# Kernel optimization log

Hardware: AMD Instinct MI355X
Metric: run time of the kernel (lower is better)

## Reference

```python
import jax, jax.numpy as jnp
import numpy as np
from jax import lax

B, C, H, W, K = 64, 64, 128, 128, 4
EPS = 1e-5

def setup_inputs() -> dict:
    key = jax.random.key(0)
    ks = jax.random.split(key, 8)
    def p(i, shape, scale=0.05):
        return jax.random.normal(ks[i], shape, dtype=jnp.float32) * scale
    return {
        "rgb":   jax.random.normal(ks[0], (B, C, H, W), dtype=jnp.float32),
        "depth": jax.random.normal(ks[1], (B, C, H, W), dtype=jnp.float32),
        # kernel_gen MLP: Linear(2C->C), Linear(C -> K*C*9)
        "w1": p(2, (C, 2 * C)), "b1": jnp.zeros((C,), jnp.float32),
        "w2": p(3, (K * C * 9, C)), "b2": jnp.zeros((K * C * 9,), jnp.float32),
        # freq_decompose: Conv3x3(C->C) + BN (eval-mode stats)
        "fd_w": p(4, (C, C, 3, 3)), "fd_b": jnp.zeros((C,), jnp.float32),
        "fd_scale": jnp.ones((C,), jnp.float32), "fd_bias": jnp.zeros((C,), jnp.float32),
        "fd_mean": jnp.zeros((C,), jnp.float32), "fd_var": jnp.ones((C,), jnp.float32),
        # fusion: Conv1x1(2C->C) + BN
        "fu_w": p(5, (C, 2 * C, 1, 1)), "fu_b": jnp.zeros((C,), jnp.float32),
        "fu_scale": jnp.ones((C,), jnp.float32), "fu_bias": jnp.zeros((C,), jnp.float32),
        "fu_mean": jnp.zeros((C,), jnp.float32), "fu_var": jnp.ones((C,), jnp.float32),
    }

def _bn(x, scale, bias, mean, var):
    # eval-mode batchnorm over channel axis 1
    inv = scale / jnp.sqrt(var + EPS)
    return x * inv[None, :, None, None] + (bias - mean * inv)[None, :, None, None]

def _conv(x, w, pad):
    return lax.conv_general_dilated(x, w, (1, 1), ((pad, pad), (pad, pad)),
                                    dimension_numbers=("NCHW", "OIHW", "NCHW"))

def reference(rgb, depth, w1, b1, w2, b2,
              fd_w, fd_b, fd_scale, fd_bias, fd_mean, fd_var,
              fu_w, fu_b, fu_scale, fu_bias, fu_mean, fu_var):
    b, c, h, w = rgb.shape
    k = w2.shape[0] // (c * 9)
    # kernel generation: global avg pool over concat -> MLP
    pooled = jnp.concatenate([rgb, depth], axis=1).mean(axis=(2, 3))  # [B, 2C]
    hid = jax.nn.relu(pooled @ w1.T + b1)                             # [B, C]
    kernels = (hid @ w2.T + b2).reshape(b, k, c, 3, 3)                # [B, K, C, 3, 3]
    norms = jnp.linalg.norm(kernels.reshape(b, k, -1), axis=2)        # [B, K]
    attn = jax.nn.softmax(norms, axis=1)
    weighted_kernel = jnp.einsum("bk,bkcij->bcij", attn, kernels)     # [B, C, 3, 3]
    # NOTE: faithful to the torch code: plain conv2d with out_channels=B (requires B==C)
    dynamic_feat = _conv(rgb, weighted_kernel, 1)                     # [B, B, H, W]
    freq_feat = jax.nn.relu(_bn(_conv(depth, fd_w, 1) + fd_b[None, :, None, None],
                                fd_scale, fd_bias, fd_mean, fd_var))
    cat = jnp.concatenate([dynamic_feat, freq_feat], axis=1)          # [B, 2C, H, W]
    fused = jax.nn.relu(_bn(_conv(cat, fu_w, 0) + fu_b[None, :, None, None],
                            fu_scale, fu_bias, fu_mean, fu_var))
    return fused
```

## Files before the change

### kernel.cpp

```cpp
#include <hip/hip_runtime.h>
#include <hip/hip_bf16.h>

#define CB 64
#define HH 128
#define WW 128
#define KK 4
#define EPSV 1e-5f
#define HWSZ (HH*WW)

using f32x4   = __attribute__((ext_vector_type(4))) float;
using f32x16  = __attribute__((ext_vector_type(16))) float;
using short8  = __attribute__((ext_vector_type(8))) short;

static constexpr size_t WS_POOLED = 0;
static constexpr size_t WS_HID    = 8192;
static constexpr size_t WS_KERN   = 12288;
static constexpr size_t WS_SSQ    = 159744;
static constexpr size_t WS_WK     = 160000;
static constexpr size_t WS_EFFW   = 196864;
static constexpr size_t WS_FUW2   = 233728;
static constexpr size_t WS_FDINV  = 237824;
static constexpr size_t WS_FDBETA = 237888;
static constexpr size_t WS_FUINV  = 237952;
static constexpr size_t WS_FUBETA = 238016;
static constexpr size_t WT3_BYTE = 49152;
static constexpr size_t WFD_BYTE = 49152 + 73728;
static constexpr size_t W1_BYTE  = 49152 + 147456;
static constexpr size_t WS_PART_BYTE   = 4u << 20;
static constexpr size_t WS_DEPTHT_BYTE = 8u << 20;
static constexpr size_t WS_RGBT_BYTE   = 140u << 20;


__global__ void k_consts(const float* __restrict__ fd_scale, const float* __restrict__ fd_bias,
                         const float* __restrict__ fd_mean, const float* __restrict__ fd_var,
                         const float* __restrict__ fd_b,
                         const float* __restrict__ fu_scale, const float* __restrict__ fu_bias,
                         const float* __restrict__ fu_mean, const float* __restrict__ fu_var,
                         const float* __restrict__ fu_b,
                         float* __restrict__ ws) {
    int c = threadIdx.x;
    if (c < CB) {
        float fdi = fd_scale[c] / sqrtf(fd_var[c] + EPSV);
        ws[WS_FDINV + c]  = fdi;
        ws[WS_FDBETA + c] = (fd_b[c] - fd_mean[c]) * fdi + fd_bias[c];
        float fui = fu_scale[c] / sqrtf(fu_var[c] + EPSV);
        ws[WS_FUINV + c]  = fui;
        ws[WS_FUBETA + c] = (fu_b[c] - fu_mean[c]) * fui + fu_bias[c];
    }
}

__device__ __forceinline__ unsigned int pack_bf16(float a, float b) {
    __hip_bfloat16 ha = __float2bfloat16(a), hb = __float2bfloat16(b);
    return (unsigned int)*(unsigned short*)&ha | ((unsigned int)*(unsigned short*)&hb << 16);
}

__global__ __launch_bounds__(256) void k_nhwc(const float* __restrict__ rgb,
                                              const float* __restrict__ depth,
                                              unsigned int* __restrict__ rgbT,
                                              unsigned int* __restrict__ depthT,
                                              float* __restrict__ part) {
    int g = blockIdx.x;
    int b = blockIdx.y;
    int t = threadIdx.x;

    if (g == 64) {
        unsigned int* dR0 = rgbT   + ((size_t)b * 130 + 0)   * 130 * 32;
        unsigned int* dR1 = rgbT   + ((size_t)b * 130 + 129) * 130 * 32;
        unsigned int* dD0 = depthT + ((size_t)b * 130 + 0)   * 130 * 32;
        unsigned int* dD1 = depthT + ((size_t)b * 130 + 129) * 130 * 32;
        for (int i = t; i < 130 * 32; i += 256) {
            dR0[i] = 0u; dR1[i] = 0u; dD0[i] = 0u; dD1[i] = 0u;
        }
        return;
    }
    int y0 = g * 2;
    {
        int tensor = t >> 7, side = (t >> 6) & 1, row = (t >> 5) & 1, j = t & 31;
        unsigned int* d = tensor ? depthT : rgbT;
        d[(((size_t)b * 130 + (y0 + 1 + row)) * 130 + (side ? 129 : 0)) * 32 + j] = 0u;
    }

    __shared__ unsigned int staged[32][260];
    __shared__ float poolacc[128];
    int w = t >> 6, lane = t & 63;

    #pragma unroll
    for (int ph = 0; ph < 2; ++ph) {
        const float* src = ph ? depth : rgb;
        unsigned int* dst = ph ? depthT : rgbT;
        if (ph) __syncthreads();

        #pragma unroll
        for (int i = 0; i < 8; ++i) {
            int pair = i * 4 + w;
            int c = pair * 2;
            const float4* s0 = (const float4*)(src + ((size_t)(b * CB + c)) * HWSZ
                                               + (size_t)y0 * WW);
            const float4* s1 = (const float4*)(src + ((size_t)(b * CB + c + 1)) * HWSZ
                                               + (size_t)y0 * WW);
            float4 v0 = s0[lane];
            float4 v1 = s1[lane];
            unsigned int pk0 = pack_bf16(v0.x, v1.x);
            unsigned int pk1 = pack_bf16(v0.y, v1.y);
            unsigned int pk2 = pack_bf16(v0.z, v1.z);
            unsigned int pk3 = pack_bf16(v0.w, v1.w);
            uint4 q = {pk0, pk1, pk2, pk3};
            *(uint4*)&staged[pair][lane * 4] = q;
            float sa = v0.x + v0.y + v0.z + v0.w;
            float sb = v1.x + v1.y + v1.z + v1.w;
            #pragma unroll
            for (int off = 32; off; off >>= 1) {
                sa += __shfl_down(sa, off, 64);
                sb += __shfl_down(sb, off, 64);
            }
            if (lane == 0) {
                poolacc[ph * 64 + c]     = sa;
                poolacc[ph * 64 + c + 1] = sb;
            }
        }
        __syncthreads();

        {
            int row = t >> 7, x = t & 127;
            unsigned int line[32];
            #pragma unroll
            for (int p = 0; p < 32; ++p) line[p] = staged[p][t];
            unsigned int* dp = dst + (((size_t)b * 130 + (y0 + 1 + row)) * 130 + 1 + x) * 32;
            #pragma unroll
            for (int q = 0; q < 8; ++q)
                *(uint4*)(dp + q * 4) = *(uint4*)&line[q * 4];
        }
    }
    __syncthreads();
    if (t < 128)
        part[((size_t)b * 64 + g) * 128 + t] = poolacc[t];
}

__global__ __launch_bounds__(256) void k_pool2(const float* __restrict__ part,
                                               float* __restrict__ ws) {
    int b = blockIdx.x, t = threadIdx.x, cc = t & 127, q = t >> 7;
    float s = 0.f;
    for (int g = q * 32; g < q * 32 + 32; ++g)
        s += part[((size_t)b * 64 + g) * 128 + cc];
    __shared__ float red[2][128];
    red[q][cc] = s;
    __syncthreads();
    if (t < 128)
        ws[WS_POOLED + b * 128 + t] = (red[0][t] + red[1][t]) * (1.f / 16384.f);
}

__global__ void k_hid(const float* __restrict__ w1, const float* __restrict__ b1,
                      float* __restrict__ ws) {
    __shared__ float p[128];
    int b = blockIdx.x, j = threadIdx.x;
    p[j] = ws[WS_POOLED + b * 128 + j];
    __syncthreads();
    if (j < CB) {
        float s = b1[j];
        const float* wr = w1 + j * 128;
        #pragma unroll 8
        for (int i = 0; i < 128; ++i) s += p[i] * wr[i];
        ws[WS_HID + b * CB + j] = fmaxf(s, 0.f);
    }
}

__global__ __launch_bounds__(256) void k_kern(const float* __restrict__ w2, const float* __restrict__ b2,
                                              float* __restrict__ ws) {
    __shared__ float h[CB];
    int b = blockIdx.x, t = threadIdx.x;
    if (t < CB) h[t] = ws[WS_HID + b * CB + t];
    __syncthreads();
    float local = 0.f;
    #pragma unroll
    for (int r9 = 0; r9 < 9; ++r9) {
        int r = t * 9 + r9;
        float s = b2[r];
        const float* wr = w2 + r * CB;
        #pragma unroll 8
        for (int m = 0; m < CB; ++m) s += h[m] * wr[m];
        ws[WS_KERN + b * 2304 + r] = s;
        local += s * s;
    }
    #pragma unroll
    for (int off = 32; off; off >>= 1) local += __shfl_down(local, off, 64);
    if ((t & 63) == 0) ws[WS_SSQ + b * KK + (t >> 6)] = local;
}

__global__ __launch_bounds__(256) void k_wk(float* __restrict__ ws) {
    __shared__ float attn[KK];
    int b = blockIdx.x, t = threadIdx.x;
    if (t == 0) {
        float n[KK], m = -1e30f;
        #pragma unroll
        for (int k = 0; k < KK; ++k) { n[k] = sqrtf(ws[WS_SSQ + b * KK + k]); m = fmaxf(m, n[k]); }
        float e[KK], den = 0.f;
        #pragma unroll
        for (int k = 0; k < KK; ++k) { e[k] = expf(n[k] - m); den += e[k]; }
        float inv = 1.f / den;
        #pragma unroll
        for (int k = 0; k < KK; ++k) attn[k] = e[k] * inv;
    }
    __syncthreads();
    const float* kb = ws + WS_KERN + b * 2304;
    float a0 = attn[0], a1 = attn[1], a2 = attn[2], a3 = attn[3];
    for (int idx = t; idx < 576; idx += 256) {
        float s = a0 * kb[idx] + a1 * kb[576 + idx] + a2 * kb[1152 + idx] + a3 * kb[1728 + idx];
        ws[WS_WK + b * 576 + idx] = s;
    }
}

__global__ __launch_bounds__(256) void k_effw(const float* __restrict__ fu_w, float* __restrict__ ws) {
    int o = blockIdx.x, t = threadIdx.x;
    __shared__ float fw[CB];
    float fi = ws[WS_FUINV + o];
    if (t < CB) {
        fw[t] = fu_w[o * 128 + t] * fi;
        ws[WS_FUW2 + o * CB + t] = fu_w[o * 128 + CB + t] * fi;
    }
    __syncthreads();
    for (int idx = t; idx < 576; idx += 256) {
        float s = 0.f;
        #pragma unroll 8
        for (int c = 0; c < CB; ++c) s += fw[c] * ws[WS_WK + c * 576 + idx];
        ws[WS_EFFW + o * 576 + idx] = s;
    }
}

__global__ void k_prepw(const float* __restrict__ fd_w, float* __restrict__ ws) {
    int e = blockIdx.x * 256 + threadIdx.x;
    unsigned short* wt3 = (unsigned short*)((char*)ws + WT3_BYTE);
    unsigned short* wfd = (unsigned short*)((char*)ws + WFD_BYTE);
    unsigned short* w1o = (unsigned short*)((char*)ws + W1_BYTE);
    if (e < 73728) {
        int set = (e >= 36864) ? 1 : 0;
        int e2 = set ? e - 36864 : e;
        int j = e2 & 7, l = (e2 >> 3) & 63, oh = (e2 >> 9) & 1, Kq = (e2 >> 10) & 3, tap = e2 >> 12;
        int och = oh * 32 + (l & 31);
        int cin = Kq * 16 + (l >> 5) * 8 + j;
        float v = set ? fd_w[(och * 64 + cin) * 9 + tap] * ws[WS_FDINV + och]
                      : ws[WS_EFFW + och * 576 + cin * 9 + tap];
        __hip_bfloat16 h = __float2bfloat16(v);
        (set ? wfd : wt3)[e2] = *(unsigned short*)&h;
    } else if (e < 77824) {
        int e3 = e - 73728;
        int j = e3 & 7, l = (e3 >> 3) & 63, oh = (e3 >> 9) & 1, Kq = e3 >> 10;
        int och = oh * 32 + (l & 31);
        int cin = Kq * 16 + (l >> 5) * 8 + j;
        __hip_bfloat16 h = __float2bfloat16(ws[WS_FUW2 + och * CB + cin]);
        w1o[e3] = *(unsigned short*)&h;
    }
}


__device__ __forceinline__ void gload_lds16(const void* g, void* l) {
    __builtin_amdgcn_global_load_lds((const __attribute__((address_space(1))) unsigned int*)g,
                                     (__attribute__((address_space(3))) unsigned int*)l, 16, 0, 0);
}

__device__ __forceinline__ void stage_async(const unsigned short* __restrict__ T, int b,
                                            int y0p, int x0p, int t, char* tile) {
    const char* base = (const char*)(T + (((size_t)b * 130 + y0p) * 130 + x0p) * 64);
    #pragma unroll
    for (int it = 0; it < 10; ++it) {
        int n = it * 256 + t;
        int row = n / 272, rem = n - row * 272;
        int xx = rem >> 3, cs = rem & 7;
        gload_lds16(base + (size_t)row * 16640 + xx * 128 + ((cs ^ (xx & 7)) << 4),
                    tile + n * 16);
    }
    if (t < 160) {
        int n = 2560 + t;
        int row = n / 272, rem = n - row * 272;
        int xx = rem >> 3, cs = rem & 7;
        gload_lds16(base + (size_t)row * 16640 + xx * 128 + ((cs ^ (xx & 7)) << 4),
                    tile + n * 16);
    }
}

__device__ __forceinline__ void conv3x3w2(f32x16 (&acc)[2][2], const unsigned short* __restrict__ Wt,
                                          const char* tile, int w, int lane) {
    int px = lane & 31, hi = lane >> 5;
    #pragma unroll
    for (int tap = 0; tap < 9; ++tap) {
        const int di = tap / 3, dj = tap % 3;
        short8 wa[2][4];
        #pragma unroll
        for (int Kq = 0; Kq < 4; ++Kq)
            #pragma unroll
            for (int oh = 0; oh < 2; ++oh)
                wa[oh][Kq] = *(const short8*)(Wt + ((((tap * 4 + Kq) * 2 + oh) * 64 + lane) << 3));
        const int xx = px + dj;
        #pragma unroll
        for (int pxg = 0; pxg < 2; ++pxg) {
            const char* base = tile + (w * 2 + pxg + di) * 4352 + xx * 128;
            #pragma unroll
            for (int Kq = 0; Kq < 4; ++Kq) {
                short8 bf = *(const short8*)(base + (((Kq * 2 + hi) ^ (xx & 7)) << 4));
                __builtin_amdgcn_s_setprio(1);
                acc[0][pxg] = __builtin_amdgcn_mfma_f32_32x32x16_bf16(wa[0][Kq], bf, acc[0][pxg], 0, 0, 0);
                acc[1][pxg] = __builtin_amdgcn_mfma_f32_32x32x16_bf16(wa[1][Kq], bf, acc[1][pxg], 0, 0, 0);
                __builtin_amdgcn_s_setprio(0);
            }
        }
    }
}

__global__ __launch_bounds__(256, 2) void k_fused(const unsigned short* __restrict__ rgbT,
                                                  const unsigned short* __restrict__ depthT,
                                                  const float* __restrict__ ws,
                                                  float* __restrict__ out) {
    __shared__ __align__(16) char tile[43520];
    int b = blockIdx.z;
    int x0 = blockIdx.x * 32, y0 = blockIdx.y * 8;
    int t = threadIdx.x, lane = t & 63, w = t >> 6;
    int px = lane & 31, hi = lane >> 5;

    const unsigned short* wfd = (const unsigned short*)((const char*)ws + WFD_BYTE);
    const unsigned short* wt3 = (const unsigned short*)((const char*)ws + WT3_BYTE);
    const unsigned short* w1o = (const unsigned short*)((const char*)ws + W1_BYTE);

    stage_async(depthT, b, y0, x0, t, tile);

    f32x16 facc[2][2];
    #pragma unroll
    for (int oh = 0; oh < 2; ++oh) {
        f32x16 bi;
        #pragma unroll
        for (int r = 0; r < 16; ++r)
            bi[r] = ws[WS_FDBETA + oh * 32 + (r & 3) + 8 * (r >> 2) + 4 * hi];
        facc[oh][0] = bi;
        facc[oh][1] = bi;
    }
    __syncthreads();

    conv3x3w2(facc, wfd, tile, w, lane);
    __syncthreads();

    {
        unsigned int* fl = (unsigned int*)tile;
        #pragma unroll
        for (int oh = 0; oh < 2; ++oh)
            #pragma unroll
            for (int pxg = 0; pxg < 2; ++pxg) {
                int p = (w * 2 + pxg) * 32 + px;
                #pragma unroll
                for (int q = 0; q < 4; ++q) {
                    unsigned int u0 = pack_bf16(fmaxf(facc[oh][pxg][q * 4 + 0], 0.f),
                                                fmaxf(facc[oh][pxg][q * 4 + 1], 0.f));
                    unsigned int u1 = pack_bf16(fmaxf(facc[oh][pxg][q * 4 + 2], 0.f),
                                                fmaxf(facc[oh][pxg][q * 4 + 3], 0.f));
                    int slot = (q + oh * 4) ^ (p & 7);
                    int dw = p * 32 + slot * 4 + hi * 2;
                    fl[dw] = u0;
                    fl[dw + 1] = u1;
                }
            }
    }
    __syncthreads();

    f32x16 acc[2][2];
    #pragma unroll
    for (int oh = 0; oh < 2; ++oh) {
        f32x16 bi;
        #pragma unroll
        for (int r = 0; r < 16; ++r)
            bi[r] = ws[WS_FUBETA + oh * 32 + (r & 3) + 8 * (r >> 2) + 4 * hi];
        acc[oh][0] = bi;
        acc[oh][1] = bi;
    }
    #pragma unroll
    for (int Kq = 0; Kq < 4; ++Kq) {
        short8 w1a[2];
        #pragma unroll
        for (int oh = 0; oh < 2; ++oh)
            w1a[oh] = *(const short8*)(w1o + (((Kq * 2 + oh) * 64 + lane) << 3));
        #pragma unroll
        for (int pxg = 0; pxg < 2; ++pxg) {
            int p = (w * 2 + pxg) * 32 + px;
            short8 bf = *(const short8*)(tile + p * 128 + (((Kq * 2 + hi) ^ (p & 7)) << 4));
            __builtin_amdgcn_s_setprio(1);
            acc[0][pxg] = __builtin_amdgcn_mfma_f32_32x32x16_bf16(w1a[0], bf, acc[0][pxg], 0, 0, 0);
            acc[1][pxg] = __builtin_amdgcn_mfma_f32_32x32x16_bf16(w1a[1], bf, acc[1][pxg], 0, 0, 0);
            __builtin_amdgcn_s_setprio(0);
        }
    }
    __syncthreads();

    stage_async(rgbT, b, y0, x0, t, tile);
    __syncthreads();

    conv3x3w2(acc, wt3, tile, w, lane);
    __syncthreads();

    float* slab = (float*)(tile + w * 8704);
    #pragma unroll
    for (int pxg = 0; pxg < 2; ++pxg) {
        #pragma unroll
        for (int oh = 0; oh < 2; ++oh)
            #pragma unroll
            for (int q = 0; q < 4; ++q)
                #pragma unroll
                for (int i = 0; i < 4; ++i)
                    slab[(oh * 32 + q * 8 + hi * 4 + i) * 33 + px] =
                        fmaxf(acc[oh][pxg][q * 4 + i], 0.f);
        int y = y0 + w * 2 + pxg;
        #pragma unroll
        for (int c2 = 0; c2 < 32; ++c2) {
            int c = c2 * 2 + hi;
            out[(size_t)(b * CB + c) * HWSZ + (size_t)y * WW + x0 + px] = slab[c * 33 + px];
        }
    }
}


extern "C" void kernel_launch(void* const* d_in, const int* in_sizes, int n_in,
                              void* d_out, int out_size, void* d_ws, size_t ws_size,
                              hipStream_t stream) {
    const float* rgb      = (const float*)d_in[0];
    const float* depth    = (const float*)d_in[1];
    const float* w1       = (const float*)d_in[2];
    const float* b1       = (const float*)d_in[3];
    const float* w2       = (const float*)d_in[4];
    const float* b2       = (const float*)d_in[5];
    const float* fd_w     = (const float*)d_in[6];
    const float* fd_b     = (const float*)d_in[7];
    const float* fd_scale = (const float*)d_in[8];
    const float* fd_bias  = (const float*)d_in[9];
    const float* fd_mean  = (const float*)d_in[10];
    const float* fd_var   = (const float*)d_in[11];
    const float* fu_w     = (const float*)d_in[12];
    const float* fu_b     = (const float*)d_in[13];
    const float* fu_scale = (const float*)d_in[14];
    const float* fu_bias  = (const float*)d_in[15];
    const float* fu_mean  = (const float*)d_in[16];
    const float* fu_var   = (const float*)d_in[17];

    float* ws = (float*)d_ws;
    float* part = (float*)((char*)d_ws + WS_PART_BYTE);
    unsigned int* depthT = (unsigned int*)((char*)d_ws + WS_DEPTHT_BYTE);
    unsigned int* rgbT   = (unsigned int*)((char*)d_ws + WS_RGBT_BYTE);
    float* out = (float*)d_out;

    k_consts<<<1, 64, 0, stream>>>(fd_scale, fd_bias, fd_mean, fd_var, fd_b,
                                   fu_scale, fu_bias, fu_mean, fu_var, fu_b, ws);
    k_nhwc<<<dim3(65, 64), 256, 0, stream>>>(rgb, depth, rgbT, depthT, part);
    k_pool2<<<CB, 256, 0, stream>>>(part, ws);
    k_hid<<<CB, 128, 0, stream>>>(w1, b1, ws);
    k_kern<<<CB, 256, 0, stream>>>(w2, b2, ws);
    k_wk<<<CB, 256, 0, stream>>>(ws);
    k_effw<<<CB, 256, 0, stream>>>(fu_w, ws);
    k_prepw<<<304, 256, 0, stream>>>(fd_w, ws);

    dim3 grid(WW / 32, HH / 8, CB);
    k_fused<<<grid, 256, 0, stream>>>((const unsigned short*)rgbT,
                                      (const unsigned short*)depthT, ws, out);
}
```

Baseline: 420.9 us.

## Fuse tiny MLP kernels and reuse LDS row loads across 3x3 taps

Merges the pool-reduce and hidden-layer kernels into one launch, and the kernel-generation and attention-weighting kernels into another, keeping intermediates in shared memory instead of the workspace. This removes two launches and some global round-trips. The 3x3 MFMA conv loop is reordered to iterate over dj and Kq, loading four LDS rows once and reusing them across the three vertical taps and both pixel groups. This cuts LDS reads per MFMA, at the cost of more live weight registers, which may raise register pressure under the 2-blocks-per-CU launch bound.

```diff
diff --git a/kernel.cpp b/kernel.cpp
--- a/kernel.cpp
+++ b/kernel.cpp
@@ -136,37 +136,36 @@
         part[((size_t)b * 64 + g) * 128 + t] = poolacc[t];
 }
 
-__global__ __launch_bounds__(256) void k_pool2(const float* __restrict__ part,
-                                               float* __restrict__ ws) {
+__global__ __launch_bounds__(256) void k_poolhid(const float* __restrict__ part,
+                                                 const float* __restrict__ w1,
+                                                 const float* __restrict__ b1,
+                                                 float* __restrict__ ws) {
     int b = blockIdx.x, t = threadIdx.x, cc = t & 127, q = t >> 7;
     float s = 0.f;
     for (int g = q * 32; g < q * 32 + 32; ++g)
         s += part[((size_t)b * 64 + g) * 128 + cc];
     __shared__ float red[2][128];
+    __shared__ float p[128];
     red[q][cc] = s;
     __syncthreads();
-    if (t < 128)
-        ws[WS_POOLED + b * 128 + t] = (red[0][t] + red[1][t]) * (1.f / 16384.f);
-}
-
-__global__ void k_hid(const float* __restrict__ w1, const float* __restrict__ b1,
-                      float* __restrict__ ws) {
-    __shared__ float p[128];
-    int b = blockIdx.x, j = threadIdx.x;
-    p[j] = ws[WS_POOLED + b * 128 + j];
-    __syncthreads();
-    if (j < CB) {
-        float s = b1[j];
-        const float* wr = w1 + j * 128;
+    if (t < 128) p[t] = (red[0][t] + red[1][t]) * (1.f / 16384.f);
+    __syncthreads();
+    if (t < CB) {
+        float s2 = b1[t];
+        const float* wr = w1 + t * 128;
         #pragma unroll 8
-        for (int i = 0; i < 128; ++i) s += p[i] * wr[i];
-        ws[WS_HID + b * CB + j] = fmaxf(s, 0.f);
-    }
-}
-
-__global__ __launch_bounds__(256) void k_kern(const float* __restrict__ w2, const float* __restrict__ b2,
-                                              float* __restrict__ ws) {
+        for (int i = 0; i < 128; ++i) s2 += p[i] * wr[i];
+        ws[WS_HID + b * CB + t] = fmaxf(s2, 0.f);
+    }
+}
+
+__global__ __launch_bounds__(256) void k_kernwk(const float* __restrict__ w2,
+                                                const float* __restrict__ b2,
+                                                float* __restrict__ ws) {
     __shared__ float h[CB];
+    __shared__ float kernL[2304];
+    __shared__ float attn[KK];
+    __shared__ float ssq[KK];
     int b = blockIdx.x, t = threadIdx.x;
     if (t < CB) h[t] = ws[WS_HID + b * CB + t];
     __syncthreads();
@@ -178,21 +177,17 @@
         const float* wr = w2 + r * CB;
         #pragma unroll 8
         for (int m = 0; m < CB; ++m) s += h[m] * wr[m];
-        ws[WS_KERN + b * 2304 + r] = s;
+        kernL[r] = s;
         local += s * s;
     }
     #pragma unroll
     for (int off = 32; off; off >>= 1) local += __shfl_down(local, off, 64);
-    if ((t & 63) == 0) ws[WS_SSQ + b * KK + (t >> 6)] = local;
-}
-
-__global__ __launch_bounds__(256) void k_wk(float* __restrict__ ws) {
-    __shared__ float attn[KK];
-    int b = blockIdx.x, t = threadIdx.x;
+    if ((t & 63) == 0) ssq[t >> 6] = local;
+    __syncthreads();
     if (t == 0) {
         float n[KK], m = -1e30f;
         #pragma unroll
-        for (int k = 0; k < KK; ++k) { n[k] = sqrtf(ws[WS_SSQ + b * KK + k]); m = fmaxf(m, n[k]); }
+        for (int k = 0; k < KK; ++k) { n[k] = sqrtf(ssq[k]); m = fmaxf(m, n[k]); }
         float e[KK], den = 0.f;
         #pragma unroll
         for (int k = 0; k < KK; ++k) { e[k] = expf(n[k] - m); den += e[k]; }
@@ -201,10 +196,10 @@
         for (int k = 0; k < KK; ++k) attn[k] = e[k] * inv;
     }
     __syncthreads();
-    const float* kb = ws + WS_KERN + b * 2304;
     float a0 = attn[0], a1 = attn[1], a2 = attn[2], a3 = attn[3];
     for (int idx = t; idx < 576; idx += 256) {
-        float s = a0 * kb[idx] + a1 * kb[576 + idx] + a2 * kb[1152 + idx] + a3 * kb[1728 + idx];
+        float s = a0 * kernL[idx] + a1 * kernL[576 + idx]
+                + a2 * kernL[1152 + idx] + a3 * kernL[1728 + idx];
         ws[WS_WK + b * 576 + idx] = s;
     }
 }
@@ -281,26 +276,32 @@
                                           const char* tile, int w, int lane) {
     int px = lane & 31, hi = lane >> 5;
     #pragma unroll
-    for (int tap = 0; tap < 9; ++tap) {
-        const int di = tap / 3, dj = tap % 3;
-        short8 wa[2][4];
-        #pragma unroll
-        for (int Kq = 0; Kq < 4; ++Kq)
-            #pragma unroll
-            for (int oh = 0; oh < 2; ++oh)
-                wa[oh][Kq] = *(const short8*)(Wt + ((((tap * 4 + Kq) * 2 + oh) * 64 + lane) << 3));
+    for (int dj = 0; dj < 3; ++dj) {
         const int xx = px + dj;
-        #pragma unroll
-        for (int pxg = 0; pxg < 2; ++pxg) {
-            const char* base = tile + (w * 2 + pxg + di) * 4352 + xx * 128;
-            #pragma unroll
-            for (int Kq = 0; Kq < 4; ++Kq) {
-                short8 bf = *(const short8*)(base + (((Kq * 2 + hi) ^ (xx & 7)) << 4));
-                __builtin_amdgcn_s_setprio(1);
-                acc[0][pxg] = __builtin_amdgcn_mfma_f32_32x32x16_bf16(wa[0][Kq], bf, acc[0][pxg], 0, 0, 0);
-                acc[1][pxg] = __builtin_amdgcn_mfma_f32_32x32x16_bf16(wa[1][Kq], bf, acc[1][pxg], 0, 0, 0);
-                __builtin_amdgcn_s_setprio(0);
-            }
+        const char* bbase = tile + xx * 128;
+        #pragma unroll
+        for (int Kq = 0; Kq < 4; ++Kq) {
+            short8 wa[3][2];
+            #pragma unroll
+            for (int di = 0; di < 3; ++di)
+                #pragma unroll
+                for (int oh = 0; oh < 2; ++oh)
+                    wa[di][oh] = *(const short8*)(Wt +
+                        (((((di * 3 + dj) * 4 + Kq) * 2 + oh) * 64 + lane) << 3));
+            const int so = ((Kq * 2 + hi) ^ (xx & 7)) << 4;
+            short8 r[4];
+            #pragma unroll
+            for (int j = 0; j < 4; ++j)
+                r[j] = *(const short8*)(bbase + (size_t)(w * 2 + j) * 4352 + so);
+            __builtin_amdgcn_s_setprio(1);
+            #pragma unroll
+            for (int di = 0; di < 3; ++di)
+                #pragma unroll
+                for (int pxg = 0; pxg < 2; ++pxg) {
+                    acc[0][pxg] = __builtin_amdgcn_mfma_f32_32x32x16_bf16(wa[di][0], r[di + pxg], acc[0][pxg], 0, 0, 0);
+                    acc[1][pxg] = __builtin_amdgcn_mfma_f32_32x32x16_bf16(wa[di][1], r[di + pxg], acc[1][pxg], 0, 0, 0);
+                }
+            __builtin_amdgcn_s_setprio(0);
         }
     }
 }
@@ -444,10 +445,8 @@
     k_consts<<<1, 64, 0, stream>>>(fd_scale, fd_bias, fd_mean, fd_var, fd_b,
                                    fu_scale, fu_bias, fu_mean, fu_var, fu_b, ws);
     k_nhwc<<<dim3(65, 64), 256, 0, stream>>>(rgb, depth, rgbT, depthT, part);
-    k_pool2<<<CB, 256, 0, stream>>>(part, ws);
-    k_hid<<<CB, 128, 0, stream>>>(w1, b1, ws);
-    k_kern<<<CB, 256, 0, stream>>>(w2, b2, ws);
-    k_wk<<<CB, 256, 0, stream>>>(ws);
+    k_poolhid<<<CB, 256, 0, stream>>>(part, w1, b1, ws);
+    k_kernwk<<<CB, 256, 0, stream>>>(w2, b2, ws);
     k_effw<<<CB, 256, 0, stream>>>(fu_w, ws);
     k_prepw<<<304, 256, 0, stream>>>(fd_w, ws);
 
```

After: 425.2 us. About the same (+1.0%).
